# Optimization experiments

Hardware: AMD Instinct MI355X
Metric: run time of the kernel (lower is better)

Reference implementation:

```python
import jax, jax.numpy as jnp
import numpy as np

B, N, D = 32, 1024, 256

def setup_inputs() -> dict:
    key = jax.random.key(0)
    ks = jax.random.split(key, 7)
    s = 1.0 / np.sqrt(D)
    return {
        "traj": jax.random.normal(ks[0], (B, N, D), dtype=jnp.float32),
        "Wq": jax.random.normal(ks[1], (D, D), dtype=jnp.float32) * s,
        "bq": jax.random.normal(ks[2], (D,), dtype=jnp.float32) * s,
        "Wk": jax.random.normal(ks[3], (D, D), dtype=jnp.float32) * s,
        "bk": jax.random.normal(ks[4], (D,), dtype=jnp.float32) * s,
        "Wv": jax.random.normal(ks[5], (D, D), dtype=jnp.float32) * s,
        "bv": jax.random.normal(ks[6], (D,), dtype=jnp.float32) * s,
    }

def reference(traj, Wq, bq, Wk, bk, Wv, bv):
    # torch nn.Linear: y = x @ W.T + b
    q = jnp.einsum('bnd,ed->bne', traj, Wq) + bq  # [B,N,D]
    k = jnp.einsum('bnd,ed->bne', traj, Wk) + bk  # [B,N,D]
    v = jnp.einsum('bnd,ed->bne', traj, Wv) + bv  # [B,N,D]
    # unscaled dot-product attention (original sums broadcasted Q*K over D)
    scores = jnp.einsum('bnd,bmd->bnm', q, k)     # [B,N,N]
    attn = jax.nn.softmax(scores, axis=-1)        # [B,N,N]
    out = jnp.einsum('bnm,bmd->bnd', attn, v)     # [B,N,D]
    return out
```

## Files before the change

kernel.cpp:

```cpp
#include <hip/hip_runtime.h>

#define NN 1024
#define DD 256

typedef __attribute__((ext_vector_type(8))) _Float16 f16x8;
typedef __attribute__((ext_vector_type(4))) float f32x4;

union H8 { f16x8 v; _Float16 s[8]; };

__global__ void wconv_kernel(const float* __restrict__ Wq, const float* __restrict__ Wk,
                             const float* __restrict__ Wv, _Float16* __restrict__ whf) {
  int idx = blockIdx.x * 256 + threadIdx.x;
  int e = idx >> 8, d = idx & 255;
  const float* W = (e < 256) ? Wq : (e < 512 ? Wk : Wv);
  whf[idx] = (_Float16)W[(e & 255) * 256 + d];
}

__global__ __launch_bounds__(256, 2) void proj_kernel(
    const float* __restrict__ traj,
    const float* __restrict__ bq, const float* __restrict__ bk, const float* __restrict__ bv,
    const _Float16* __restrict__ whf,
    _Float16* __restrict__ qhf, _Float16* __restrict__ khf,
    _Float16* __restrict__ vthf)
{
  __shared__ _Float16 Ws[32 * 264];
  __shared__ _Float16 Cs[64 * 88];

  const int t = threadIdx.x;
  const int lane = t & 63, wave = t >> 6;
  const int col16 = lane & 15, quad = lane >> 4;
  const int mbase = blockIdx.x * 64;

  f16x8 aq[8];
  {
    const float* ap = traj + (size_t)(mbase + wave * 16 + col16) * DD;
    for (int kk = 0; kk < 8; ++kk) {
      float4 u0 = *(const float4*)(ap + kk * 32 + quad * 8);
      float4 u1 = *(const float4*)(ap + kk * 32 + quad * 8 + 4);
      H8 xx;
      xx.s[0] = (_Float16)u0.x; xx.s[1] = (_Float16)u0.y;
      xx.s[2] = (_Float16)u0.z; xx.s[3] = (_Float16)u0.w;
      xx.s[4] = (_Float16)u1.x; xx.s[5] = (_Float16)u1.y;
      xx.s[6] = (_Float16)u1.z; xx.s[7] = (_Float16)u1.w;
      aq[kk] = xx.v;
    }
  }

  f32x4 acc[4];
  const f32x4 zero = {0.f, 0.f, 0.f, 0.f};

  for (int et = 0; et < 12; ++et) {
    for (int h = 0; h < 2; ++h) {
      __syncthreads();
      {
        int row = t >> 3;
        const _Float16* wsrc = whf + (size_t)(et * 64 + h * 32 + row) * 256;
        for (int i = 0; i < 4; ++i) {
          int c = (t & 7) + i * 8;
          *(int4*)&Ws[row * 264 + c * 8] = *(const int4*)(wsrc + c * 8);
        }
      }
      __syncthreads();
      if (h == 0) { acc[0] = zero; acc[1] = zero; acc[2] = zero; acc[3] = zero; }
      for (int kk = 0; kk < 8; ++kk)
        for (int n2 = 0; n2 < 2; ++n2) {
          f16x8 bw = *(const f16x8*)&Ws[(n2 * 16 + col16) * 264 + kk * 32 + quad * 8];
          acc[h * 2 + n2] =
              __builtin_amdgcn_mfma_f32_16x16x32_f16(aq[kk], bw, acc[h * 2 + n2], 0, 0, 0);
        }
    }
    int ebase = et * 64;
    int sel = ebase >> 8;
    const float* bias = (sel == 0) ? bq : (sel == 1 ? bk : bv);
    for (int nt = 0; nt < 4; ++nt) {
      float bvl = bias[(ebase & 255) + nt * 16 + col16];
      acc[nt][0] += bvl; acc[nt][1] += bvl; acc[nt][2] += bvl; acc[nt][3] += bvl;
    }
    if (sel < 2) {
      for (int nt = 0; nt < 4; ++nt)
        for (int r = 0; r < 4; ++r)
          Cs[(wave * 16 + quad * 4 + r) * 88 + nt * 16 + col16] = (_Float16)acc[nt][r];
      __syncthreads();
      _Float16* dst = (sel == 0) ? qhf : khf;
      int row = t >> 2;
      int colg = ebase & 255;
      for (int i = 0; i < 2; ++i) {
        int c = (t & 3) + i * 4;
        *(int4*)(dst + (size_t)(mbase + row) * 256 + colg + c * 8) =
            *(const int4*)&Cs[row * 88 + c * 8];
      }
    } else {
      for (int nt = 0; nt < 4; ++nt)
        for (int r = 0; r < 4; ++r)
          Cs[(nt * 16 + col16) * 88 + (wave * 16 + quad * 4 + r)] = (_Float16)acc[nt][r];
      __syncthreads();
      int trow = t >> 2;
      int dglob = (ebase - 512) + trow;
      int bb = mbase >> 10;
      int mloc = mbase & 1023;
      for (int i = 0; i < 2; ++i) {
        int c = (t & 3) + i * 4;
        *(int4*)(vthf + ((size_t)bb * 256 + dglob) * NN + mloc + c * 8) =
            *(const int4*)&Cs[trow * 88 + c * 8];
      }
    }
  }
}

__global__ __launch_bounds__(256, 2) void attn_kernel(
    const _Float16* __restrict__ qhf, const _Float16* __restrict__ khf,
    const _Float16* __restrict__ vthf, float* __restrict__ out)
{
  __shared__ _Float16 Ks[64 * 264];
  __shared__ _Float16 VTs[128 * 72];
  __shared__ _Float16 Ps[64 * 88];

  const int t = threadIdx.x;
  const int lane = t & 63, wave = t >> 6;
  const int col16 = lane & 15, quad = lane >> 4;
  const int qt = blockIdx.x, b = blockIdx.y;
  const int qrow0 = b * NN + qt * 64;

  f16x8 aq[8];
  {
    const _Float16* qp = qhf + (size_t)(qrow0 + wave * 16 + col16) * DD;
    for (int kk = 0; kk < 8; ++kk)
      aq[kk] = *(const f16x8*)(qp + kk * 32 + quad * 8);
  }

  float m_i[4], l_i[4], alpha[4];
  f32x4 O[16];
  const f32x4 zero = {0.f, 0.f, 0.f, 0.f};
  for (int r = 0; r < 4; ++r) { m_i[r] = -3.0e38f; l_i[r] = 0.f; }
  for (int dt = 0; dt < 16; ++dt) O[dt] = zero;

  const _Float16* kbase = khf + (size_t)(b * NN) * DD;
  const _Float16* vbase = vthf + (size_t)b * DD * NN;

  for (int kt = 0; kt < 16; ++kt) {
    __syncthreads();
    {
      int row = t >> 2;
      const _Float16* ks = kbase + (size_t)(kt * 64 + row) * DD;
      for (int i = 0; i < 8; ++i) {
        int c = (t & 3) + i * 4;
        *(int4*)&Ks[row * 264 + c * 8] = *(const int4*)(ks + c * 8);
      }
    }
    for (int g = 0; g < 2; ++g) {
      int dr = g * 64 + (t >> 2);
      const _Float16* vs = vbase + (size_t)dr * NN + kt * 64;
      for (int i = 0; i < 2; ++i) {
        int c = (t & 3) + i * 4;
        *(int4*)&VTs[dr * 72 + c * 8] = *(const int4*)(vs + c * 8);
      }
    }
    __syncthreads();

    f32x4 S[4]; S[0] = zero; S[1] = zero; S[2] = zero; S[3] = zero;
    for (int kk = 0; kk < 8; ++kk)
      for (int nt = 0; nt < 4; ++nt) {
        f16x8 bk_ = *(const f16x8*)&Ks[(nt * 16 + col16) * 264 + kk * 32 + quad * 8];
        S[nt] = __builtin_amdgcn_mfma_f32_16x16x32_f16(aq[kk], bk_, S[nt], 0, 0, 0);
      }

    for (int r = 0; r < 4; ++r) {
      float vmax = fmaxf(fmaxf(S[0][r], S[1][r]), fmaxf(S[2][r], S[3][r]));
      vmax = fmaxf(vmax, __shfl_xor(vmax, 1));
      vmax = fmaxf(vmax, __shfl_xor(vmax, 2));
      vmax = fmaxf(vmax, __shfl_xor(vmax, 4));
      vmax = fmaxf(vmax, __shfl_xor(vmax, 8));
      float nm = fmaxf(m_i[r], vmax);
      alpha[r] = __expf(m_i[r] - nm);
      float rs = 0.f;
      for (int nt = 0; nt < 4; ++nt) {
        float pv = __expf(S[nt][r] - nm);
        S[nt][r] = pv;
        rs += pv;
      }
      rs += __shfl_xor(rs, 1);
      rs += __shfl_xor(rs, 2);
      rs += __shfl_xor(rs, 4);
      rs += __shfl_xor(rs, 8);
      l_i[r] = l_i[r] * alpha[r] + rs;
      m_i[r] = nm;
    }
    for (int dt = 0; dt < 16; ++dt)
      for (int r = 0; r < 4; ++r) O[dt][r] *= alpha[r];

    for (int nt = 0; nt < 4; ++nt)
      for (int r = 0; r < 4; ++r)
        Ps[(wave * 16 + quad * 4 + r) * 88 + nt * 16 + col16] = (_Float16)S[nt][r];
    f16x8 ap[2];
    for (int k2 = 0; k2 < 2; ++k2)
      ap[k2] = *(const f16x8*)&Ps[(wave * 16 + col16) * 88 + k2 * 32 + quad * 8];

    for (int dt = 0; dt < 8; ++dt)
      for (int k2 = 0; k2 < 2; ++k2) {
        f16x8 bv_ = *(const f16x8*)&VTs[(dt * 16 + col16) * 72 + k2 * 32 + quad * 8];
        O[dt] = __builtin_amdgcn_mfma_f32_16x16x32_f16(ap[k2], bv_, O[dt], 0, 0, 0);
      }
    __syncthreads();
    for (int g = 0; g < 2; ++g) {
      int dr = g * 64 + (t >> 2);
      const _Float16* vs = vbase + (size_t)(128 + dr) * NN + kt * 64;
      for (int i = 0; i < 2; ++i) {
        int c = (t & 3) + i * 4;
        *(int4*)&VTs[dr * 72 + c * 8] = *(const int4*)(vs + c * 8);
      }
    }
    __syncthreads();
    for (int dt = 0; dt < 8; ++dt)
      for (int k2 = 0; k2 < 2; ++k2) {
        f16x8 bv_ = *(const f16x8*)&VTs[(dt * 16 + col16) * 72 + k2 * 32 + quad * 8];
        O[8 + dt] = __builtin_amdgcn_mfma_f32_16x16x32_f16(ap[k2], bv_, O[8 + dt], 0, 0, 0);
      }
  }

  for (int r = 0; r < 4; ++r) {
    float inv = 1.0f / l_i[r];
    float* orow = out + (size_t)(qrow0 + wave * 16 + quad * 4 + r) * DD;
    for (int dt = 0; dt < 16; ++dt)
      orow[dt * 16 + col16] = O[dt][r] * inv;
  }
}

extern "C" void kernel_launch(void* const* d_in, const int* in_sizes, int n_in,
                              void* d_out, int out_size, void* d_ws, size_t ws_size,
                              hipStream_t stream) {
  const float* traj = (const float*)d_in[0];
  const float* Wq   = (const float*)d_in[1];
  const float* bq   = (const float*)d_in[2];
  const float* Wk   = (const float*)d_in[3];
  const float* bk   = (const float*)d_in[4];
  const float* Wv   = (const float*)d_in[5];
  const float* bv   = (const float*)d_in[6];

  _Float16* qhf  = (_Float16*)d_ws;
  _Float16* khf  = qhf  + (size_t)32768 * 256;
  _Float16* vthf = khf  + (size_t)32768 * 256;
  _Float16* whf  = vthf + (size_t)32768 * 256;

  wconv_kernel<<<768, 256, 0, stream>>>(Wq, Wk, Wv, whf);
  proj_kernel<<<512, 256, 0, stream>>>(traj, bq, bk, bv, whf, qhf, khf, vthf);
  attn_kernel<<<dim3(16, 32), 256, 0, stream>>>(qhf, khf, vthf, (float*)d_out);
}
```

Baseline: 196.9 us.

## Load K, V and weight MFMA operands directly from global, drop LDS staging

Both the projection and attention kernels stop staging weights, K and V^T tiles in shared memory. Each wave now loads its MFMA B-operands straight from global memory and relies on L1/L2 caching for reuse across the four waves. This removes the LDS copies and most of the __syncthreads barriers, and the smaller LDS footprint lets the launch bounds ask for 4 and 3 blocks per CU. In exchange the four waves of a block read the same data redundantly from cache, and the per-lane 16-byte global loads are strided (rows 512 B apart for K and weights, 2 KB apart for V^T), which risks exposed memory latency inside the MFMA loops.

```diff
diff --git a/kernel.cpp b/kernel.cpp
--- a/kernel.cpp
+++ b/kernel.cpp
@@ -16,14 +16,13 @@
   whf[idx] = (_Float16)W[(e & 255) * 256 + d];
 }
 
-__global__ __launch_bounds__(256, 2) void proj_kernel(
+__global__ __launch_bounds__(256, 4) void proj_kernel(
     const float* __restrict__ traj,
     const float* __restrict__ bq, const float* __restrict__ bk, const float* __restrict__ bv,
     const _Float16* __restrict__ whf,
     _Float16* __restrict__ qhf, _Float16* __restrict__ khf,
     _Float16* __restrict__ vthf)
 {
-  __shared__ _Float16 Ws[32 * 264];
   __shared__ _Float16 Cs[64 * 88];
 
   const int t = threadIdx.x;
@@ -46,29 +45,18 @@
     }
   }
 
-  f32x4 acc[4];
   const f32x4 zero = {0.f, 0.f, 0.f, 0.f};
 
   for (int et = 0; et < 12; ++et) {
-    for (int h = 0; h < 2; ++h) {
-      __syncthreads();
-      {
-        int row = t >> 3;
-        const _Float16* wsrc = whf + (size_t)(et * 64 + h * 32 + row) * 256;
-        for (int i = 0; i < 4; ++i) {
-          int c = (t & 7) + i * 8;
-          *(int4*)&Ws[row * 264 + c * 8] = *(const int4*)(wsrc + c * 8);
-        }
-      }
-      __syncthreads();
-      if (h == 0) { acc[0] = zero; acc[1] = zero; acc[2] = zero; acc[3] = zero; }
-      for (int kk = 0; kk < 8; ++kk)
-        for (int n2 = 0; n2 < 2; ++n2) {
-          f16x8 bw = *(const f16x8*)&Ws[(n2 * 16 + col16) * 264 + kk * 32 + quad * 8];
-          acc[h * 2 + n2] =
-              __builtin_amdgcn_mfma_f32_16x16x32_f16(aq[kk], bw, acc[h * 2 + n2], 0, 0, 0);
-        }
-    }
+    f32x4 acc[4];
+    acc[0] = zero; acc[1] = zero; acc[2] = zero; acc[3] = zero;
+    const _Float16* wb = whf + (size_t)et * 64 * 256;
+    for (int kk = 0; kk < 8; ++kk)
+      for (int nt = 0; nt < 4; ++nt) {
+        f16x8 bw = *(const f16x8*)(wb + (nt * 16 + col16) * 256 + kk * 32 + quad * 8);
+        acc[nt] = __builtin_amdgcn_mfma_f32_16x16x32_f16(aq[kk], bw, acc[nt], 0, 0, 0);
+      }
+
     int ebase = et * 64;
     int sel = ebase >> 8;
     const float* bias = (sel == 0) ? bq : (sel == 1 ? bk : bv);
@@ -76,6 +64,7 @@
       float bvl = bias[(ebase & 255) + nt * 16 + col16];
       acc[nt][0] += bvl; acc[nt][1] += bvl; acc[nt][2] += bvl; acc[nt][3] += bvl;
     }
+    __syncthreads();
     if (sel < 2) {
       for (int nt = 0; nt < 4; ++nt)
         for (int r = 0; r < 4; ++r)
@@ -107,12 +96,10 @@
   }
 }
 
-__global__ __launch_bounds__(256, 2) void attn_kernel(
+__global__ __launch_bounds__(256, 3) void attn_kernel(
     const _Float16* __restrict__ qhf, const _Float16* __restrict__ khf,
     const _Float16* __restrict__ vthf, float* __restrict__ out)
 {
-  __shared__ _Float16 Ks[64 * 264];
-  __shared__ _Float16 VTs[128 * 72];
   __shared__ _Float16 Ps[64 * 88];
 
   const int t = threadIdx.x;
@@ -138,29 +125,11 @@
   const _Float16* vbase = vthf + (size_t)b * DD * NN;
 
   for (int kt = 0; kt < 16; ++kt) {
-    __syncthreads();
-    {
-      int row = t >> 2;
-      const _Float16* ks = kbase + (size_t)(kt * 64 + row) * DD;
-      for (int i = 0; i < 8; ++i) {
-        int c = (t & 3) + i * 4;
-        *(int4*)&Ks[row * 264 + c * 8] = *(const int4*)(ks + c * 8);
-      }
-    }
-    for (int g = 0; g < 2; ++g) {
-      int dr = g * 64 + (t >> 2);
-      const _Float16* vs = vbase + (size_t)dr * NN + kt * 64;
-      for (int i = 0; i < 2; ++i) {
-        int c = (t & 3) + i * 4;
-        *(int4*)&VTs[dr * 72 + c * 8] = *(const int4*)(vs + c * 8);
-      }
-    }
-    __syncthreads();
-
     f32x4 S[4]; S[0] = zero; S[1] = zero; S[2] = zero; S[3] = zero;
+    const _Float16* kb = kbase + (size_t)(kt * 64) * DD;
     for (int kk = 0; kk < 8; ++kk)
       for (int nt = 0; nt < 4; ++nt) {
-        f16x8 bk_ = *(const f16x8*)&Ks[(nt * 16 + col16) * 264 + kk * 32 + quad * 8];
+        f16x8 bk_ = *(const f16x8*)(kb + (nt * 16 + col16) * 256 + kk * 32 + quad * 8);
         S[nt] = __builtin_amdgcn_mfma_f32_16x16x32_f16(aq[kk], bk_, S[nt], 0, 0, 0);
       }
 
@@ -195,25 +164,11 @@
     for (int k2 = 0; k2 < 2; ++k2)
       ap[k2] = *(const f16x8*)&Ps[(wave * 16 + col16) * 88 + k2 * 32 + quad * 8];
 
-    for (int dt = 0; dt < 8; ++dt)
+    for (int dt = 0; dt < 16; ++dt)
       for (int k2 = 0; k2 < 2; ++k2) {
-        f16x8 bv_ = *(const f16x8*)&VTs[(dt * 16 + col16) * 72 + k2 * 32 + quad * 8];
+        f16x8 bv_ = *(const f16x8*)(vbase + (size_t)(dt * 16 + col16) * NN +
+                                    kt * 64 + k2 * 32 + quad * 8);
         O[dt] = __builtin_amdgcn_mfma_f32_16x16x32_f16(ap[k2], bv_, O[dt], 0, 0, 0);
-      }
-    __syncthreads();
-    for (int g = 0; g < 2; ++g) {
-      int dr = g * 64 + (t >> 2);
-      const _Float16* vs = vbase + (size_t)(128 + dr) * NN + kt * 64;
-      for (int i = 0; i < 2; ++i) {
-        int c = (t & 3) + i * 4;
-        *(int4*)&VTs[dr * 72 + c * 8] = *(const int4*)(vs + c * 8);
-      }
-    }
-    __syncthreads();
-    for (int dt = 0; dt < 8; ++dt)
-      for (int k2 = 0; k2 < 2; ++k2) {
-        f16x8 bv_ = *(const f16x8*)&VTs[(dt * 16 + col16) * 72 + k2 * 32 + quad * 8];
-        O[8 + dt] = __builtin_amdgcn_mfma_f32_16x16x32_f16(ap[k2], bv_, O[8 + dt], 0, 0, 0);
       }
   }
 
```

Measured after the change: 455.6 us. 131% more time.
